# Kernel tuning notes

Measured on AMD Instinct MI355X. Metric: run time of the kernel, lower is better.

## Reference

```python
import jax, jax.numpy as jnp
import numpy as np


def setup_inputs() -> dict:
    key = jax.random.key(0)
    k1, k2, k3 = jax.random.split(key, 3)
    B, L, D, H = 8, 1024, 768, 128
    text = jax.random.normal(k1, (B, L, D), dtype=jnp.float32)
    mask = jnp.ones((B, L), dtype=jnp.float32)  # accepted by forward but unused
    # nn.Linear-style init scale
    W0 = jax.random.normal(k2, (H, D), dtype=jnp.float32) / np.sqrt(D)
    b0 = jnp.zeros((H,), dtype=jnp.float32)
    W1 = jax.random.normal(k3, (1, 2 * H), dtype=jnp.float32) / np.sqrt(2 * H)
    b1 = jnp.zeros((1,), dtype=jnp.float32)
    return {"text": text, "mask": mask, "W0": W0, "b0": b0, "W1": W1, "b1": b1}


def reference(text, mask, W0, b0, W1, b1):
    # h = relu(linear0(text))  -> [B, L, 128]
    h = jax.nn.relu(jnp.einsum('bld,hd->blh', text, W0) + b0)
    H = W0.shape[0]
    # linear([h_i ; h_j]) = h_i @ w_a + h_j @ w_b + b  (split the 256->1 weight)
    w_a = W1[0, :H]   # weights applied to the row (i) copy
    w_b = W1[0, H:]   # weights applied to the column (j) copy
    s1 = jnp.einsum('blh,h->bl', h, w_a)  # [B, L]
    s2 = jnp.einsum('blh,h->bl', h, w_b)  # [B, L]
    # logits[b, i, j] = sigmoid(s1[b, i] + s2[b, j] + b1)
    logits = jax.nn.sigmoid(s1[:, :, None] + s2[:, None, :] + b1[0])
    return logits
```

## Files before the change

### kernel.cpp

```cpp
#include <hip/hip_runtime.h>

#define M_ROWS 8192
#define DIM    768
#define HCH    128

typedef __bf16 bf16x8 __attribute__((ext_vector_type(8)));
typedef float  f32x4  __attribute__((ext_vector_type(4)));

__device__ __forceinline__ unsigned short f2bf(float f) {
    union { float f; unsigned int u; } v; v.f = f;
    unsigned int u = v.u;
    u += 0x7fffu + ((u >> 16) & 1u);
    return (unsigned short)(u >> 16);
}

__global__ __launch_bounds__(256) void convert_w0_kernel(
    const float* __restrict__ W0, unsigned short* __restrict__ W0b)
{
    int i = (blockIdx.x * 256 + threadIdx.x) * 4;
    float4 v = *(const float4*)(W0 + i);
    uint2 o;
    o.x = (unsigned int)f2bf(v.x) | ((unsigned int)f2bf(v.y) << 16);
    o.y = (unsigned int)f2bf(v.z) | ((unsigned int)f2bf(v.w) << 16);
    *(uint2*)(W0b + i) = o;
}

__global__ __launch_bounds__(256) void gemm_s_kernel(
    const float* __restrict__ text,
    const unsigned short* __restrict__ W0b,
    const float* __restrict__ b0,
    const float* __restrict__ W1,
    float* __restrict__ s1, float* __restrict__ s2)
{
    __shared__ unsigned short As[32][40];
    __shared__ unsigned short Bs[128][40];
    __shared__ float red1[32][2];
    __shared__ float red2[32][2];

    const int tid  = threadIdx.x;
    const int lane = tid & 63;
    const int wave = tid >> 6;
    const int row0 = blockIdx.x * 32;

    const int wrow = (wave >> 1) * 16;
    const int wcol = (wave & 1) * 64;
    const int n16  = lane & 15;
    const int quad = lane >> 4;

    const int am  = tid >> 3;
    const int ak4 = (tid & 7) << 2;
    const int bn  = tid >> 2;
    const int bp  = tid & 3;

    const float*          aptr  = text + (size_t)(row0 + am) * DIM + ak4;
    const unsigned short* bptr0 = W0b + (size_t)bn * DIM + bp * 8;
    const unsigned short* bptr1 = bptr0 + (size_t)64 * DIM;

    f32x4 acc[4];
    #pragma unroll
    for (int j = 0; j < 4; ++j) acc[j] = (f32x4){0.f, 0.f, 0.f, 0.f};

    float4 av  = *(const float4*)aptr;
    uint4  bv0 = *(const uint4*)bptr0;
    uint4  bv1 = *(const uint4*)bptr1;

    for (int kt = 0; kt < DIM; kt += 32) {
        const int ktn = (kt + 32 < DIM) ? (kt + 32) : 0;
        float4 av_n  = *(const float4*)(aptr + ktn);
        uint4  bv0_n = *(const uint4*)(bptr0 + ktn);
        uint4  bv1_n = *(const uint4*)(bptr1 + ktn);

        uint2 o;
        o.x = (unsigned int)f2bf(av.x) | ((unsigned int)f2bf(av.y) << 16);
        o.y = (unsigned int)f2bf(av.z) | ((unsigned int)f2bf(av.w) << 16);
        *(uint2*)&As[am][ak4]         = o;
        *(uint4*)&Bs[bn][bp * 8]      = bv0;
        *(uint4*)&Bs[bn + 64][bp * 8] = bv1;
        __syncthreads();

        bf16x8 a   = *(const bf16x8*)&As[wrow + n16][quad * 8];
        bf16x8 bf0 = *(const bf16x8*)&Bs[wcol +  0 + n16][quad * 8];
        bf16x8 bf1 = *(const bf16x8*)&Bs[wcol + 16 + n16][quad * 8];
        bf16x8 bf2 = *(const bf16x8*)&Bs[wcol + 32 + n16][quad * 8];
        bf16x8 bf3 = *(const bf16x8*)&Bs[wcol + 48 + n16][quad * 8];
        acc[0] = __builtin_amdgcn_mfma_f32_16x16x32_bf16(a, bf0, acc[0], 0, 0, 0);
        acc[1] = __builtin_amdgcn_mfma_f32_16x16x32_bf16(a, bf1, acc[1], 0, 0, 0);
        acc[2] = __builtin_amdgcn_mfma_f32_16x16x32_bf16(a, bf2, acc[2], 0, 0, 0);
        acc[3] = __builtin_amdgcn_mfma_f32_16x16x32_bf16(a, bf3, acc[3], 0, 0, 0);
        __syncthreads();

        av = av_n; bv0 = bv0_n; bv1 = bv1_n;
    }

    float p1[4] = {0.f, 0.f, 0.f, 0.f};
    float p2[4] = {0.f, 0.f, 0.f, 0.f};
    #pragma unroll
    for (int j = 0; j < 4; ++j) {
        const int col = wcol + j * 16 + n16;
        const float bb = b0[col];
        const float wa = W1[col];
        const float wb = W1[HCH + col];
        #pragma unroll
        for (int r = 0; r < 4; ++r) {
            float h = acc[j][r] + bb;
            h = fmaxf(h, 0.f);
            p1[r] += h * wa;
            p2[r] += h * wb;
        }
    }
    #pragma unroll
    for (int r = 0; r < 4; ++r) {
        #pragma unroll
        for (int m = 8; m >= 1; m >>= 1) {
            p1[r] += __shfl_xor(p1[r], m);
            p2[r] += __shfl_xor(p2[r], m);
        }
    }
    if (n16 == 0) {
        #pragma unroll
        for (int r = 0; r < 4; ++r) {
            const int rr = wrow + quad * 4 + r;
            red1[rr][wave & 1] = p1[r];
            red2[rr][wave & 1] = p2[r];
        }
    }
    __syncthreads();
    if (tid < 32) {
        s1[row0 + tid] = red1[tid][0] + red1[tid][1];
        s2[row0 + tid] = red2[tid][0] + red2[tid][1];
    }
}

__global__ __launch_bounds__(256) void outer_sigmoid_kernel(
    const float* __restrict__ s1, const float* __restrict__ s2,
    const float* __restrict__ b1, float* __restrict__ out)
{
    const int bi = blockIdx.x;
    const int b  = bi >> 10;
    const float base = s1[bi] + b1[0];
    const float4 t = ((const float4*)(s2 + (b << 10)))[threadIdx.x];
    float4 r;
    r.x = 1.f / (1.f + __expf(-(base + t.x)));
    r.y = 1.f / (1.f + __expf(-(base + t.y)));
    r.z = 1.f / (1.f + __expf(-(base + t.z)));
    r.w = 1.f / (1.f + __expf(-(base + t.w)));
    ((float4*)out)[((size_t)bi << 8) + threadIdx.x] = r;
}

extern "C" void kernel_launch(void* const* d_in, const int* in_sizes, int n_in,
                              void* d_out, int out_size, void* d_ws, size_t ws_size,
                              hipStream_t stream)
{
    const float* text = (const float*)d_in[0];
    const float* W0 = (const float*)d_in[2];
    const float* b0 = (const float*)d_in[3];
    const float* W1 = (const float*)d_in[4];
    const float* b1 = (const float*)d_in[5];
    float* out = (float*)d_out;

    unsigned short* W0b = (unsigned short*)d_ws;
    float* s1 = (float*)((char*)d_ws + (size_t)HCH * DIM * sizeof(unsigned short));
    float* s2 = s1 + M_ROWS;

    convert_w0_kernel<<<96, 256, 0, stream>>>(W0, W0b);
    gemm_s_kernel<<<256, 256, 0, stream>>>(text, W0b, b0, W1, s1, s2);
    outer_sigmoid_kernel<<<8192, 256, 0, stream>>>(s1, s2, b1, out);
}
```

Measured before the change: 101.8 us.

## Fuse W0 bf16 conversion into GEMM and widen block to 512 threads

```diff
diff --git a/kernel.cpp b/kernel.cpp
--- a/kernel.cpp
+++ b/kernel.cpp
@@ -7,95 +7,85 @@
 typedef __bf16 bf16x8 __attribute__((ext_vector_type(8)));
 typedef float  f32x4  __attribute__((ext_vector_type(4)));
 
-__device__ __forceinline__ unsigned short f2bf(float f) {
+__device__ __forceinline__ unsigned int f2bf(float f) {
     union { float f; unsigned int u; } v; v.f = f;
     unsigned int u = v.u;
     u += 0x7fffu + ((u >> 16) & 1u);
-    return (unsigned short)(u >> 16);
+    return u >> 16;
 }
 
-__global__ __launch_bounds__(256) void convert_w0_kernel(
-    const float* __restrict__ W0, unsigned short* __restrict__ W0b)
-{
-    int i = (blockIdx.x * 256 + threadIdx.x) * 4;
-    float4 v = *(const float4*)(W0 + i);
-    uint2 o;
-    o.x = (unsigned int)f2bf(v.x) | ((unsigned int)f2bf(v.y) << 16);
-    o.y = (unsigned int)f2bf(v.z) | ((unsigned int)f2bf(v.w) << 16);
-    *(uint2*)(W0b + i) = o;
+__device__ __forceinline__ uint4 pack8(const float4 a, const float4 b) {
+    uint4 o;
+    o.x = f2bf(a.x) | (f2bf(a.y) << 16);
+    o.y = f2bf(a.z) | (f2bf(a.w) << 16);
+    o.z = f2bf(b.x) | (f2bf(b.y) << 16);
+    o.w = f2bf(b.z) | (f2bf(b.w) << 16);
+    return o;
 }
 
-__global__ __launch_bounds__(256) void gemm_s_kernel(
+__global__ __launch_bounds__(512) void gemm_s_kernel(
     const float* __restrict__ text,
-    const unsigned short* __restrict__ W0b,
+    const float* __restrict__ W0,
     const float* __restrict__ b0,
     const float* __restrict__ W1,
     float* __restrict__ s1, float* __restrict__ s2)
 {
     __shared__ unsigned short As[32][40];
     __shared__ unsigned short Bs[128][40];
-    __shared__ float red1[32][2];
-    __shared__ float red2[32][2];
+    __shared__ float red1[32][4];
+    __shared__ float red2[32][4];
 
     const int tid  = threadIdx.x;
     const int lane = tid & 63;
     const int wave = tid >> 6;
     const int row0 = blockIdx.x * 32;
 
-    const int wrow = (wave >> 1) * 16;
-    const int wcol = (wave & 1) * 64;
+    const int wrow = (wave >> 2) * 16;
+    const int wcol = (wave & 3) * 32;
     const int n16  = lane & 15;
     const int quad = lane >> 4;
 
-    const int am  = tid >> 3;
-    const int ak4 = (tid & 7) << 2;
-    const int bn  = tid >> 2;
-    const int bp  = tid & 3;
+    const int srow = tid >> 2;
+    const int sk8  = (tid & 3) * 8;
+    const float* bptr = W0   + (size_t)srow * DIM + sk8;
+    const float* aptr = text + (size_t)(row0 + (srow & 31)) * DIM + sk8;
+    const bool doA = (tid < 128);
 
-    const float*          aptr  = text + (size_t)(row0 + am) * DIM + ak4;
-    const unsigned short* bptr0 = W0b + (size_t)bn * DIM + bp * 8;
-    const unsigned short* bptr1 = bptr0 + (size_t)64 * DIM;
+    f32x4 acc[2];
+    acc[0] = (f32x4){0.f, 0.f, 0.f, 0.f};
+    acc[1] = (f32x4){0.f, 0.f, 0.f, 0.f};
 
-    f32x4 acc[4];
-    #pragma unroll
-    for (int j = 0; j < 4; ++j) acc[j] = (f32x4){0.f, 0.f, 0.f, 0.f};
-
-    float4 av  = *(const float4*)aptr;
-    uint4  bv0 = *(const uint4*)bptr0;
-    uint4  bv1 = *(const uint4*)bptr1;
+    float4 bA = *(const float4*)bptr;
+    float4 bB = *(const float4*)(bptr + 4);
+    float4 aA, aB;
+    if (doA) { aA = *(const float4*)aptr; aB = *(const float4*)(aptr + 4); }
 
     for (int kt = 0; kt < DIM; kt += 32) {
         const int ktn = (kt + 32 < DIM) ? (kt + 32) : 0;
-        float4 av_n  = *(const float4*)(aptr + ktn);
-        uint4  bv0_n = *(const uint4*)(bptr0 + ktn);
-        uint4  bv1_n = *(const uint4*)(bptr1 + ktn);
+        float4 nbA = *(const float4*)(bptr + ktn);
+        float4 nbB = *(const float4*)(bptr + ktn + 4);
+        float4 naA, naB;
+        if (doA) { naA = *(const float4*)(aptr + ktn); naB = *(const float4*)(aptr + ktn + 4); }
 
-        uint2 o;
-        o.x = (unsigned int)f2bf(av.x) | ((unsigned int)f2bf(av.y) << 16);
-        o.y = (unsigned int)f2bf(av.z) | ((unsigned int)f2bf(av.w) << 16);
-        *(uint2*)&As[am][ak4]         = o;
-        *(uint4*)&Bs[bn][bp * 8]      = bv0;
-        *(uint4*)&Bs[bn + 64][bp * 8] = bv1;
+        *(uint4*)&Bs[srow][sk8] = pack8(bA, bB);
+        if (doA) *(uint4*)&As[srow & 31][sk8] = pack8(aA, aB);
         __syncthreads();
 
         bf16x8 a   = *(const bf16x8*)&As[wrow + n16][quad * 8];
         bf16x8 bf0 = *(const bf16x8*)&Bs[wcol +  0 + n16][quad * 8];
         bf16x8 bf1 = *(const bf16x8*)&Bs[wcol + 16 + n16][quad * 8];
-        bf16x8 bf2 = *(const bf16x8*)&Bs[wcol + 32 + n16][quad * 8];
-        bf16x8 bf3 = *(const bf16x8*)&Bs[wcol + 48 + n16][quad * 8];
         acc[0] = __builtin_amdgcn_mfma_f32_16x16x32_bf16(a, bf0, acc[0], 0, 0, 0);
         acc[1] = __builtin_amdgcn_mfma_f32_16x16x32_bf16(a, bf1, acc[1], 0, 0, 0);
-        acc[2] = __builtin_amdgcn_mfma_f32_16x16x32_bf16(a, bf2, acc[2], 0, 0, 0);
-        acc[3] = __builtin_amdgcn_mfma_f32_16x16x32_bf16(a, bf3, acc[3], 0, 0, 0);
         __syncthreads();
 
-        av = av_n; bv0 = bv0_n; bv1 = bv1_n;
+        bA = nbA; bB = nbB;
+        if (doA) { aA = naA; aB = naB; }
     }
 
     float p1[4] = {0.f, 0.f, 0.f, 0.f};
     float p2[4] = {0.f, 0.f, 0.f, 0.f};
     #pragma unroll
-    for (int j = 0; j < 4; ++j) {
+    for (int j = 0; j < 2; ++j) {
         const int col = wcol + j * 16 + n16;
         const float bb = b0[col];
         const float wa = W1[col];
@@ -120,14 +110,14 @@
         #pragma unroll
         for (int r = 0; r < 4; ++r) {
             const int rr = wrow + quad * 4 + r;
-            red1[rr][wave & 1] = p1[r];
-            red2[rr][wave & 1] = p2[r];
+            red1[rr][wave & 3] = p1[r];
+            red2[rr][wave & 3] = p2[r];
         }
     }
     __syncthreads();
     if (tid < 32) {
-        s1[row0 + tid] = red1[tid][0] + red1[tid][1];
-        s2[row0 + tid] = red2[tid][0] + red2[tid][1];
+        s1[row0 + tid] = red1[tid][0] + red1[tid][1] + red1[tid][2] + red1[tid][3];
+        s2[row0 + tid] = red2[tid][0] + red2[tid][1] + red2[tid][2] + red2[tid][3];
     }
 }
 
@@ -158,11 +148,9 @@
     const float* b1 = (const float*)d_in[5];
     float* out = (float*)d_out;
 
-    unsigned short* W0b = (unsigned short*)d_ws;
-    float* s1 = (float*)((char*)d_ws + (size_t)HCH * DIM * sizeof(unsigned short));
+    float* s1 = (float*)d_ws;
     float* s2 = s1 + M_ROWS;
 
-    convert_w0_kernel<<<96, 256, 0, stream>>>(W0, W0b);
-    gemm_s_kernel<<<256, 256, 0, stream>>>(text, W0b, b0, W1, s1, s2);
+    gemm_s_kernel<<<256, 512, 0, stream>>>(text, W0, b0, W1, s1, s2);
     outer_sigmoid_kernel<<<8192, 256, 0, stream>>>(s1, s2, b1, out);
 }
```

Measured after the change: 103.5 us. About the same (+1.7%).
